# Optimization experiments

Measured on AMD Instinct MI355X. Metric: run time of the kernel, lower is better.

## Reference

```python
import jax, jax.numpy as jnp
import numpy as np

D_MODEL = 512
N_HEADS = 8
HEAD_DIM = D_MODEL // N_HEADS  # 64


def setup_inputs() -> dict:
    key = jax.random.key(0)
    ks = jax.random.split(key, 12)
    B, SQ, SK = 4, 2048, 2048
    s = 1.0 / np.sqrt(D_MODEL)
    return {
        "query": jax.random.normal(ks[0], (B, SQ, D_MODEL), jnp.float32),
        "key": jax.random.normal(ks[1], (B, SK, D_MODEL), jnp.float32),
        "value": jax.random.normal(ks[2], (B, SK, D_MODEL), jnp.float32),
        "Wq": jax.random.normal(ks[3], (D_MODEL, D_MODEL), jnp.float32) * s,
        "bq": jnp.zeros((D_MODEL,), jnp.float32),
        "Wk": jax.random.normal(ks[4], (D_MODEL, D_MODEL), jnp.float32) * s,
        "bk": jnp.zeros((D_MODEL,), jnp.float32),
        "Wv": jax.random.normal(ks[5], (D_MODEL, D_MODEL), jnp.float32) * s,
        "bv": jnp.zeros((D_MODEL,), jnp.float32),
        "Wo": jax.random.normal(ks[6], (D_MODEL, D_MODEL), jnp.float32) * s,
        "bo": jnp.zeros((D_MODEL,), jnp.float32),
    }


def reference(query, key, value, Wq, bq, Wk, bk, Wv, bv, Wo, bo):
    B, SQ, _ = query.shape
    SK = key.shape[1]
    # QKV projections
    Q = query @ Wq.T + bq  # [B,SQ,D]
    K = key @ Wk.T + bk    # [B,SK,D]
    V = value @ Wv.T + bv  # [B,SK,D]
    # split heads -> [B,H,S,hd]
    Q = Q.reshape(B, SQ, N_HEADS, HEAD_DIM).transpose(0, 2, 1, 3)
    K = K.reshape(B, SK, N_HEADS, HEAD_DIM).transpose(0, 2, 1, 3)
    V = V.reshape(B, SK, N_HEADS, HEAD_DIM).transpose(0, 2, 1, 3)
    scale = jnp.sqrt(jnp.float32(HEAD_DIM))
    scores = jnp.einsum('bhqd,bhkd->bhqk', Q, K) / scale  # [B,H,SQ,SK]
    attn = jax.nn.softmax(scores, axis=-1)  # dropout p=0 (eval)
    ctx = jnp.einsum('bhqk,bhkd->bhqd', attn, V)
    ctx = ctx.transpose(0, 2, 1, 3).reshape(B, SQ, D_MODEL)
    # exact (erf) GELU as in torch F.gelu default
    out = jax.nn.gelu(ctx, approximate=False) @ Wo.T + bo
    return out
```

## Files before the change

### kernel.cpp

```cpp
#include <hip/hip_runtime.h>
#include <hip/hip_bf16.h>

#define D_MODEL 512
#define N_HEADS 8
#define HEAD_DIM 64
#define BATCH 4
#define SEQ 2048

typedef _Float16 f16;
typedef _Float16 f16x8 __attribute__((ext_vector_type(8)));
typedef _Float16 f16x4 __attribute__((ext_vector_type(4)));
typedef float f32x4 __attribute__((ext_vector_type(4)));
typedef unsigned int u32x4 __attribute__((ext_vector_type(4)));

#define MFMA16(a, b, c) __builtin_amdgcn_mfma_f32_16x16x32_f16((a), (b), (c), 0, 0, 0)

#define GLOAD_LDS16(src, dst)                                                   \
    __builtin_amdgcn_global_load_lds(                                           \
        (const __attribute__((address_space(1))) void*)(src),                   \
        (__attribute__((address_space(3))) void*)(dst), 16, 0, 0)

#if __has_builtin(__builtin_amdgcn_exp2f)
#define EXP2(x) __builtin_amdgcn_exp2f(x)
#else
#define EXP2(x) __expf((x) * 0.6931471805599453f)
#endif

#define QSCALE 0.18033688011112042f
#define OFF2 8.656170245333781f

__global__ __launch_bounds__(256) void wsplit(
    const float* __restrict__ w0, const float* __restrict__ w1,
    const float* __restrict__ w2, const float* __restrict__ w3,
    f16* __restrict__ h0, f16* __restrict__ h1,
    f16* __restrict__ h2, f16* __restrict__ h3)
{
    const int j = blockIdx.y;
    const float* s = (j == 0) ? w0 : (j == 1) ? w1 : (j == 2) ? w2 : w3;
    f16* dh = (j == 0) ? h0 : (j == 1) ? h1 : (j == 2) ? h2 : h3;
    const int n4 = (D_MODEL * D_MODEL) >> 2;
    for (int i = blockIdx.x * 256 + threadIdx.x; i < n4; i += gridDim.x * 256) {
        float4 x = ((const float4*)s)[i];
        f16x4 hv = {(f16)x.x, (f16)x.y, (f16)x.z, (f16)x.w};
        ((f16x4*)dh)[i] = hv;
    }
}

__global__ __launch_bounds__(256, 3) void proj_mfma(
    const float* __restrict__ Xq, const float* __restrict__ Xk,
    const float* __restrict__ Xv,
    const f16* __restrict__ Wqh, const f16* __restrict__ Wkh,
    const f16* __restrict__ Wvh,
    const float* __restrict__ bq, const float* __restrict__ bk,
    const float* __restrict__ bv,
    f16* __restrict__ Qh, f16* __restrict__ Kh, f16* __restrict__ Vt)
{
    __shared__ f16 ldsA[128 * 64];
    __shared__ f16 ldsW[128 * 64];

    const int z = blockIdx.z;
    const float* X = (z == 0) ? Xq : (z == 1) ? Xk : Xv;
    const f16* Wh = (z == 0) ? Wqh : (z == 1) ? Wkh : Wvh;
    const float* bias = (z == 0) ? bq : (z == 1) ? bk : bv;

    const int m0 = blockIdx.x * 128;
    const int n0 = blockIdx.y * 128;

    const int tid = threadIdx.x;
    const int w = tid >> 6, l = tid & 63;
    const int lp = l >> 4, lq = l & 15;
    const int wm = w >> 1, wn = w & 1;

    f32x4 acc[4][4] = {};

    for (int kt = 0; kt < D_MODEL; kt += 64) {
        __syncthreads();
        float4 av[4][2];
        int arow[4], aslot[4];
#pragma unroll
        for (int j = 0; j < 4; ++j) {
            const int chunk = j * 256 + tid;
            arow[j] = chunk >> 3;
            aslot[j] = chunk & 7;
            const float* sp = X + (size_t)(m0 + arow[j]) * D_MODEL + kt + aslot[j] * 8;
            av[j][0] = *(const float4*)sp;
            av[j][1] = *(const float4*)(sp + 4);
        }
#pragma unroll
        for (int j = 0; j < 4; ++j) {
            const int cb = j * 256 + w * 64;
            const int chunk = cb + l;
            const int row = chunk >> 3;
            const int slot = (chunk & 7) ^ (row & 7);
            GLOAD_LDS16(Wh + (size_t)(n0 + row) * D_MODEL + kt + slot * 8,
                        ldsW + cb * 8);
        }
#pragma unroll
        for (int j = 0; j < 4; ++j) {
            f16x8 hv;
            hv[0] = (f16)av[j][0].x; hv[1] = (f16)av[j][0].y;
            hv[2] = (f16)av[j][0].z; hv[3] = (f16)av[j][0].w;
            hv[4] = (f16)av[j][1].x; hv[5] = (f16)av[j][1].y;
            hv[6] = (f16)av[j][1].z; hv[7] = (f16)av[j][1].w;
            *(f16x8*)(ldsA + arow[j] * 64 + ((aslot[j] ^ (arow[j] & 7)) << 3)) = hv;
        }
        __syncthreads();

        f16x8 af[4][2];
#pragma unroll
        for (int mt = 0; mt < 4; ++mt) {
            const int R = wm * 64 + mt * 16 + lq;
#pragma unroll
            for (int s = 0; s < 2; ++s)
                af[mt][s] = *(const f16x8*)(ldsA + R * 64 + (((s * 4 + lp) ^ (R & 7)) << 3));
        }
        __builtin_amdgcn_s_setprio(1);
#pragma unroll
        for (int nt = 0; nt < 4; ++nt) {
            const int R = wn * 64 + nt * 16 + lq;
            f16x8 b0 = *(const f16x8*)(ldsW + R * 64 + (((0 + lp) ^ (R & 7)) << 3));
            f16x8 b1 = *(const f16x8*)(ldsW + R * 64 + (((4 + lp) ^ (R & 7)) << 3));
#pragma unroll
            for (int mt = 0; mt < 4; ++mt) {
                acc[mt][nt] = MFMA16(af[mt][0], b0, acc[mt][nt]);
                acc[mt][nt] = MFMA16(af[mt][1], b1, acc[mt][nt]);
            }
        }
        __builtin_amdgcn_s_setprio(0);
    }

    const int m_base = m0 + wm * 64;
    const int n_base = n0 + wn * 64;
    const int b = m0 / SEQ;
    const int h = n_base >> 6;
    const size_t bh_ = (size_t)b * N_HEADS + h;

    if (z == 0) {
#pragma unroll
        for (int nt = 0; nt < 4; ++nt) {
            const int n = n_base + nt * 16 + lq;
            const float bn = bias[n];
            const int d = n & 63;
#pragma unroll
            for (int mt = 0; mt < 4; ++mt) {
#pragma unroll
                for (int r = 0; r < 4; ++r) {
                    const int s = (m_base + mt * 16 + lp * 4 + r) & (SEQ - 1);
                    Qh[(bh_ * SEQ + s) * 64 + d] = (f16)((acc[mt][nt][r] + bn) * QSCALE);
                }
            }
        }
    } else if (z == 1) {
#pragma unroll
        for (int nt = 0; nt < 4; ++nt) {
            const int n = n_base + nt * 16 + lq;
            const float bn = bias[n];
            const int d = n & 63;
#pragma unroll
            for (int mt = 0; mt < 4; ++mt) {
#pragma unroll
                for (int r = 0; r < 4; ++r) {
                    const int s = (m_base + mt * 16 + lp * 4 + r) & (SEQ - 1);
                    Kh[(bh_ * SEQ + s) * 64 + d] = (f16)(acc[mt][nt][r] + bn);
                }
            }
        }
    } else {
#pragma unroll
        for (int nt = 0; nt < 4; ++nt) {
            const int n = n_base + nt * 16 + lq;
            const float bn = bias[n];
            const int d = n & 63;
#pragma unroll
            for (int mt = 0; mt < 4; ++mt) {
                const int s0 = (m_base + mt * 16 + lp * 4) & (SEQ - 1);
                f16x4 col;
#pragma unroll
                for (int r = 0; r < 4; ++r)
                    col[r] = (f16)(acc[mt][nt][r] + bn);
                *(f16x4*)(Vt + (bh_ * 64 + d) * SEQ + s0) = col;
            }
        }
    }
}

__global__ __launch_bounds__(256, 4) void out_mfma(
    const f16* __restrict__ Gh, const f16* __restrict__ Woh,
    const float* __restrict__ bo, float* __restrict__ Out)
{
    __shared__ f16 ldsA[64 * 64];
    __shared__ f16 ldsW[128 * 64];

    const int m0 = blockIdx.x * 64;
    const int n0 = blockIdx.y * 128;

    const int tid = threadIdx.x;
    const int w = tid >> 6, l = tid & 63;
    const int lp = l >> 4, lq = l & 15;
    const int wm = w >> 1, wn = w & 1;

    f32x4 acc[2][4] = {};

    for (int kt = 0; kt < D_MODEL; kt += 64) {
        __syncthreads();
#pragma unroll
        for (int j = 0; j < 2; ++j) {
            const int cb = j * 256 + w * 64;
            const int chunk = cb + l;
            const int row = chunk >> 3;
            const int slot = (chunk & 7) ^ (row & 7);
            GLOAD_LDS16(Gh + (size_t)(m0 + row) * D_MODEL + kt + slot * 8,
                        ldsA + cb * 8);
        }
#pragma unroll
        for (int j = 0; j < 4; ++j) {
            const int cb = j * 256 + w * 64;
            const int chunk = cb + l;
            const int row = chunk >> 3;
            const int slot = (chunk & 7) ^ (row & 7);
            GLOAD_LDS16(Woh + (size_t)(n0 + row) * D_MODEL + kt + slot * 8,
                        ldsW + cb * 8);
        }
        __syncthreads();

        f16x8 af[2][2];
#pragma unroll
        for (int mt = 0; mt < 2; ++mt) {
            const int R = wm * 32 + mt * 16 + lq;
#pragma unroll
            for (int s = 0; s < 2; ++s)
                af[mt][s] = *(const f16x8*)(ldsA + R * 64 + (((s * 4 + lp) ^ (R & 7)) << 3));
        }
        __builtin_amdgcn_s_setprio(1);
#pragma unroll
        for (int nt = 0; nt < 4; ++nt) {
            const int R = wn * 64 + nt * 16 + lq;
            f16x8 b0 = *(const f16x8*)(ldsW + R * 64 + (((0 + lp) ^ (R & 7)) << 3));
            f16x8 b1 = *(const f16x8*)(ldsW + R * 64 + (((4 + lp) ^ (R & 7)) << 3));
#pragma unroll
            for (int mt = 0; mt < 2; ++mt) {
                acc[mt][nt] = MFMA16(af[mt][0], b0, acc[mt][nt]);
                acc[mt][nt] = MFMA16(af[mt][1], b1, acc[mt][nt]);
            }
        }
        __builtin_amdgcn_s_setprio(0);
    }

#pragma unroll
    for (int nt = 0; nt < 4; ++nt) {
        const int n = n0 + wn * 64 + nt * 16 + lq;
        const float bn = bo[n];
#pragma unroll
        for (int mt = 0; mt < 2; ++mt) {
#pragma unroll
            for (int r = 0; r < 4; ++r) {
                const int m = m0 + wm * 32 + mt * 16 + lp * 4 + r;
                Out[(size_t)m * D_MODEL + n] = acc[mt][nt][r] + bn;
            }
        }
    }
}

__global__ __launch_bounds__(256, 4) void flash_mfma(
    const f16* __restrict__ Qh, const f16* __restrict__ Kh,
    const f16* __restrict__ Vt, f16* __restrict__ Gh)
{
    __shared__ f16 KV[2][2][4096];

    const int tid = threadIdx.x;
    const int w  = tid >> 6;
    const int l  = tid & 63;
    const int lp = l >> 4;
    const int lq = l & 15;

    const int id = blockIdx.x;
    const int work = (id & 7) * 128 + (id >> 3);
    const int bh = work >> 5;
    const int b  = bh >> 3, h = bh & 7;
    const int qw = (work & 31) * 64 + w * 16;

    f16x8 qf[2];
#pragma unroll
    for (int s = 0; s < 2; ++s)
        qf[s] = *(const f16x8*)(Qh + ((size_t)bh * SEQ + qw + lq) * 64 + s * 32 + lp * 8);

    f16x8 ones;
#pragma unroll
    for (int i = 0; i < 8; ++i) ones[i] = (f16)1.f;

    f32x4 o[4];
#pragma unroll
    for (int c = 0; c < 4; ++c) o[c] = (f32x4){0.f, 0.f, 0.f, 0.f};
    f32x4 lf = (f32x4){0.f, 0.f, 0.f, 0.f};

    auto STAGE = [&](int k0, int bf) {
#pragma unroll
        for (int j = 0; j < 4; ++j) {
            const int gi = w + 4 * j;
            const int tset = gi >> 3;
            const int t = gi & 7;
            const int lrow = t * 8 + (l >> 3);
            const int slot = (l & 7) ^ (lrow & 7);
            if (tset == 0)
                GLOAD_LDS16(Kh + ((size_t)bh * SEQ + k0 + lrow) * 64 + slot * 8,
                            &KV[bf][0][t * 512]);
            else
                GLOAD_LDS16(Vt + ((size_t)bh * 64 + lrow) * SEQ + k0 + slot * 8,
                            &KV[bf][1][t * 512]);
        }
    };

    STAGE(0, 0);
    int buf = 0;
    const int NT = SEQ / 64;

    for (int t = 0; t < NT; ++t) {
        asm volatile("s_waitcnt vmcnt(0)" ::: "memory");
        __builtin_amdgcn_s_barrier();
        if (t < NT - 1) STAGE((t + 1) * 64, buf ^ 1);
        __builtin_amdgcn_sched_barrier(0);

        const f16* Kt_ = &KV[buf][0][0];
        const f16* Vt_ = &KV[buf][1][0];

        f32x4 st[4];
#pragma unroll
        for (int c = 0; c < 4; ++c)
            st[c] = (f32x4){-OFF2, -OFF2, -OFF2, -OFF2};
        __builtin_amdgcn_s_setprio(1);
#pragma unroll
        for (int mt = 0; mt < 4; ++mt) {
            const int krow = mt * 16 + lq;
#pragma unroll
            for (int s = 0; s < 2; ++s) {
                const int byteoff = krow * 128 + (((4 * s + lp) ^ (krow & 7)) << 4);
                f16x8 ah = *(const f16x8*)((const char*)Kt_ + byteoff);
                st[mt] = MFMA16(ah, qf[s], st[mt]);
            }
        }
        __builtin_amdgcn_s_setprio(0);

        f16x8 vbr[2][4];
#pragma unroll
        for (int s = 0; s < 2; ++s)
#pragma unroll
            for (int nt = 0; nt < 4; ++nt) {
                const int d = nt * 16 + lq;
                const int byteoff = d * 128 + (((4 * s + lp) ^ (d & 7)) << 4);
                vbr[s][nt] = *(const f16x8*)((const char*)Vt_ + byteoff);
            }

        unsigned int pk0[4], pk1[4];
#pragma unroll
        for (int mt = 0; mt < 4; ++mt) {
            float e0 = EXP2(st[mt][0]);
            float e1 = EXP2(st[mt][1]);
            float e2 = EXP2(st[mt][2]);
            float e3 = EXP2(st[mt][3]);
            pk0[mt] = __builtin_bit_cast(unsigned int,
                          __builtin_amdgcn_cvt_pkrtz(e0, e1));
            pk1[mt] = __builtin_bit_cast(unsigned int,
                          __builtin_amdgcn_cvt_pkrtz(e2, e3));
        }

        f16x8 pa[2];
#pragma unroll
        for (int s = 0; s < 2; ++s) {
            unsigned int x0 = pk0[2 * s], y0 = pk0[2 * s + 1];
            unsigned int x1 = pk1[2 * s], y1 = pk1[2 * s + 1];
            asm("v_permlane32_swap_b32 %0, %1" : "+v"(x0), "+v"(y0));
            asm("v_permlane16_swap_b32 %0, %1" : "+v"(x0), "+v"(y0));
            asm("v_permlane32_swap_b32 %0, %1" : "+v"(x1), "+v"(y1));
            asm("v_permlane16_swap_b32 %0, %1" : "+v"(x1), "+v"(y1));
            u32x4 t4 = {x0, x1, y0, y1};
            pa[s] = __builtin_bit_cast(f16x8, t4);
        }

        __builtin_amdgcn_s_setprio(1);
#pragma unroll
        for (int s = 0; s < 2; ++s) {
            lf = MFMA16(pa[s], ones, lf);
#pragma unroll
            for (int nt = 0; nt < 4; ++nt)
                o[nt] = MFMA16(pa[s], vbr[s][nt], o[nt]);
        }
        __builtin_amdgcn_s_setprio(0);

        buf ^= 1;
    }

#pragma unroll
    for (int j = 0; j < 4; ++j) {
        const float inv = 1.f / lf[j];
        const int row = qw + lp * 4 + j;
#pragma unroll
        for (int nt = 0; nt < 4; ++nt) {
            float x = o[nt][j] * inv;
            float g = 0.5f * x * (1.f + erff(x * 0.70710678118654752f));
            Gh[((size_t)(b * SEQ + row)) * D_MODEL + h * 64 + nt * 16 + lq] = (f16)g;
        }
    }
}

extern "C" void kernel_launch(void* const* d_in, const int* in_sizes, int n_in,
                              void* d_out, int out_size, void* d_ws, size_t ws_size,
                              hipStream_t stream)
{
    const float* query = (const float*)d_in[0];
    const float* key   = (const float*)d_in[1];
    const float* value = (const float*)d_in[2];
    const float* Wq = (const float*)d_in[3];
    const float* bq = (const float*)d_in[4];
    const float* Wk = (const float*)d_in[5];
    const float* bk = (const float*)d_in[6];
    const float* Wv = (const float*)d_in[7];
    const float* bv = (const float*)d_in[8];
    const float* Wo = (const float*)d_in[9];
    const float* bo = (const float*)d_in[10];

    char* ws = (char*)d_ws;
    const size_t MB = 1024 * 1024;
    const size_t KB = 1024;
    f16* Qh = (f16*)(ws + 0 * MB);
    f16* Kh = (f16*)(ws + 8 * MB);
    f16* Vt = (f16*)(ws + 16 * MB);
    f16* Gh = (f16*)(ws + 24 * MB);
    f16* Wqh = (f16*)(ws + 32 * MB);
    f16* Wkh = (f16*)(ws + 32 * MB + 512 * KB);
    f16* Wvh = (f16*)(ws + 33 * MB);
    f16* Woh = (f16*)(ws + 33 * MB + 512 * KB);

    wsplit<<<dim3(64, 4), 256, 0, stream>>>(Wq, Wk, Wv, Wo, Wqh, Wkh, Wvh, Woh);

    proj_mfma<<<dim3(BATCH * SEQ / 128, D_MODEL / 128, 3), 256, 0, stream>>>(
        query, key, value, Wqh, Wkh, Wvh, bq, bk, bv, Qh, Kh, Vt);

    flash_mfma<<<dim3(1024), 256, 0, stream>>>(Qh, Kh, Vt, Gh);

    out_mfma<<<dim3(BATCH * SEQ / 64, D_MODEL / 128), 256, 0, stream>>>(
        Gh, Woh, bo, (float*)d_out);
}
```

Baseline: 93.17 us.

## Process two 16-row query sub-tiles per wave in flash attention

Each wave now handles 32 query rows as two 16-row sub-tiles instead of 16, so a block covers 128 queries and the grid shrinks from 1024 to 512 blocks. Each K fragment and V fragment read from LDS is reused for two MFMAs, halving LDS traffic and K/V global staging per query row. In exchange, register pressure roughly doubles for accumulators, launch bounds drop to 2 blocks per SM, and fewer blocks may reduce latency hiding and load balance across the 256 CUs.

```diff
diff --git a/kernel.cpp b/kernel.cpp
--- a/kernel.cpp
+++ b/kernel.cpp
@@ -261,7 +261,7 @@
     }
 }
 
-__global__ __launch_bounds__(256, 4) void flash_mfma(
+__global__ __launch_bounds__(256, 2) void flash_mfma(
     const f16* __restrict__ Qh, const f16* __restrict__ Kh,
     const f16* __restrict__ Vt, f16* __restrict__ Gh)
 {
@@ -274,24 +274,29 @@
     const int lq = l & 15;
 
     const int id = blockIdx.x;
-    const int work = (id & 7) * 128 + (id >> 3);
-    const int bh = work >> 5;
+    const int work = (id & 7) * 64 + (id >> 3);
+    const int bh = work >> 4;
     const int b  = bh >> 3, h = bh & 7;
-    const int qw = (work & 31) * 64 + w * 16;
-
-    f16x8 qf[2];
-#pragma unroll
-    for (int s = 0; s < 2; ++s)
-        qf[s] = *(const f16x8*)(Qh + ((size_t)bh * SEQ + qw + lq) * 64 + s * 32 + lp * 8);
+    const int q0 = (work & 15) * 128 + w * 32;
+
+    f16x8 qf[2][2];
+#pragma unroll
+    for (int sub = 0; sub < 2; ++sub)
+#pragma unroll
+        for (int s = 0; s < 2; ++s)
+            qf[sub][s] = *(const f16x8*)(Qh + ((size_t)bh * SEQ + q0 + sub * 16 + lq) * 64
+                                          + s * 32 + lp * 8);
 
     f16x8 ones;
 #pragma unroll
     for (int i = 0; i < 8; ++i) ones[i] = (f16)1.f;
 
-    f32x4 o[4];
-#pragma unroll
-    for (int c = 0; c < 4; ++c) o[c] = (f32x4){0.f, 0.f, 0.f, 0.f};
-    f32x4 lf = (f32x4){0.f, 0.f, 0.f, 0.f};
+    f32x4 o[2][4];
+#pragma unroll
+    for (int sub = 0; sub < 2; ++sub)
+#pragma unroll
+        for (int c = 0; c < 4; ++c) o[sub][c] = (f32x4){0.f, 0.f, 0.f, 0.f};
+    f32x4 lf[2] = {(f32x4){0.f, 0.f, 0.f, 0.f}, (f32x4){0.f, 0.f, 0.f, 0.f}};
 
     auto STAGE = [&](int k0, int bf) {
 #pragma unroll
@@ -323,10 +328,12 @@
         const f16* Kt_ = &KV[buf][0][0];
         const f16* Vt_ = &KV[buf][1][0];
 
-        f32x4 st[4];
-#pragma unroll
-        for (int c = 0; c < 4; ++c)
-            st[c] = (f32x4){-OFF2, -OFF2, -OFF2, -OFF2};
+        f32x4 st[2][4];
+#pragma unroll
+        for (int sub = 0; sub < 2; ++sub)
+#pragma unroll
+            for (int c = 0; c < 4; ++c)
+                st[sub][c] = (f32x4){-OFF2, -OFF2, -OFF2, -OFF2};
         __builtin_amdgcn_s_setprio(1);
 #pragma unroll
         for (int mt = 0; mt < 4; ++mt) {
@@ -335,7 +342,9 @@
             for (int s = 0; s < 2; ++s) {
                 const int byteoff = krow * 128 + (((4 * s + lp) ^ (krow & 7)) << 4);
                 f16x8 ah = *(const f16x8*)((const char*)Kt_ + byteoff);
-                st[mt] = MFMA16(ah, qf[s], st[mt]);
+#pragma unroll
+                for (int sub = 0; sub < 2; ++sub)
+                    st[sub][mt] = MFMA16(ah, qf[sub][s], st[sub][mt]);
             }
         }
         __builtin_amdgcn_s_setprio(0);
@@ -350,39 +359,44 @@
                 vbr[s][nt] = *(const f16x8*)((const char*)Vt_ + byteoff);
             }
 
-        unsigned int pk0[4], pk1[4];
-#pragma unroll
-        for (int mt = 0; mt < 4; ++mt) {
-            float e0 = EXP2(st[mt][0]);
-            float e1 = EXP2(st[mt][1]);
-            float e2 = EXP2(st[mt][2]);
-            float e3 = EXP2(st[mt][3]);
-            pk0[mt] = __builtin_bit_cast(unsigned int,
-                          __builtin_amdgcn_cvt_pkrtz(e0, e1));
-            pk1[mt] = __builtin_bit_cast(unsigned int,
-                          __builtin_amdgcn_cvt_pkrtz(e2, e3));
-        }
-
-        f16x8 pa[2];
+        f16x8 pa[2][2];
+#pragma unroll
+        for (int sub = 0; sub < 2; ++sub) {
+            unsigned int pk0[4], pk1[4];
+#pragma unroll
+            for (int mt = 0; mt < 4; ++mt) {
+                float e0 = EXP2(st[sub][mt][0]);
+                float e1 = EXP2(st[sub][mt][1]);
+                float e2 = EXP2(st[sub][mt][2]);
+                float e3 = EXP2(st[sub][mt][3]);
+                pk0[mt] = __builtin_bit_cast(unsigned int,
+                              __builtin_amdgcn_cvt_pkrtz(e0, e1));
+                pk1[mt] = __builtin_bit_cast(unsigned int,
+                              __builtin_amdgcn_cvt_pkrtz(e2, e3));
+            }
+#pragma unroll
+            for (int s = 0; s < 2; ++s) {
+                unsigned int x0 = pk0[2 * s], y0 = pk0[2 * s + 1];
+                unsigned int x1 = pk1[2 * s], y1 = pk1[2 * s + 1];
+                asm("v_permlane32_swap_b32 %0, %1" : "+v"(x0), "+v"(y0));
+                asm("v_permlane16_swap_b32 %0, %1" : "+v"(x0), "+v"(y0));
+                asm("v_permlane32_swap_b32 %0, %1" : "+v"(x1), "+v"(y1));
+                asm("v_permlane16_swap_b32 %0, %1" : "+v"(x1), "+v"(y1));
+                u32x4 t4 = {x0, x1, y0, y1};
+                pa[sub][s] = __builtin_bit_cast(f16x8, t4);
+            }
+        }
+
+        __builtin_amdgcn_s_setprio(1);
 #pragma unroll
         for (int s = 0; s < 2; ++s) {
-            unsigned int x0 = pk0[2 * s], y0 = pk0[2 * s + 1];
-            unsigned int x1 = pk1[2 * s], y1 = pk1[2 * s + 1];
-            asm("v_permlane32_swap_b32 %0, %1" : "+v"(x0), "+v"(y0));
-            asm("v_permlane16_swap_b32 %0, %1" : "+v"(x0), "+v"(y0));
-            asm("v_permlane32_swap_b32 %0, %1" : "+v"(x1), "+v"(y1));
-            asm("v_permlane16_swap_b32 %0, %1" : "+v"(x1), "+v"(y1));
-            u32x4 t4 = {x0, x1, y0, y1};
-            pa[s] = __builtin_bit_cast(f16x8, t4);
-        }
-
-        __builtin_amdgcn_s_setprio(1);
-#pragma unroll
-        for (int s = 0; s < 2; ++s) {
-            lf = MFMA16(pa[s], ones, lf);
-#pragma unroll
-            for (int nt = 0; nt < 4; ++nt)
-                o[nt] = MFMA16(pa[s], vbr[s][nt], o[nt]);
+#pragma unroll
+            for (int sub = 0; sub < 2; ++sub) {
+                lf[sub] = MFMA16(pa[sub][s], ones, lf[sub]);
+#pragma unroll
+                for (int nt = 0; nt < 4; ++nt)
+                    o[sub][nt] = MFMA16(pa[sub][s], vbr[s][nt], o[sub][nt]);
+            }
         }
         __builtin_amdgcn_s_setprio(0);
 
@@ -390,14 +404,17 @@
     }
 
 #pragma unroll
-    for (int j = 0; j < 4; ++j) {
-        const float inv = 1.f / lf[j];
-        const int row = qw + lp * 4 + j;
-#pragma unroll
-        for (int nt = 0; nt < 4; ++nt) {
-            float x = o[nt][j] * inv;
-            float g = 0.5f * x * (1.f + erff(x * 0.70710678118654752f));
-            Gh[((size_t)(b * SEQ + row)) * D_MODEL + h * 64 + nt * 16 + lq] = (f16)g;
+    for (int sub = 0; sub < 2; ++sub) {
+#pragma unroll
+        for (int j = 0; j < 4; ++j) {
+            const float inv = 1.f / lf[sub][j];
+            const int row = q0 + sub * 16 + lp * 4 + j;
+#pragma unroll
+            for (int nt = 0; nt < 4; ++nt) {
+                float x = o[sub][nt][j] * inv;
+                float g = 0.5f * x * (1.f + erff(x * 0.70710678118654752f));
+                Gh[((size_t)(b * SEQ + row)) * D_MODEL + h * 64 + nt * 16 + lq] = (f16)g;
+            }
         }
     }
 }
@@ -435,7 +452,7 @@
     proj_mfma<<<dim3(BATCH * SEQ / 128, D_MODEL / 128, 3), 256, 0, stream>>>(
         query, key, value, Wqh, Wkh, Wvh, bq, bk, bv, Qh, Kh, Vt);
 
-    flash_mfma<<<dim3(1024), 256, 0, stream>>>(Qh, Kh, Vt, Gh);
+    flash_mfma<<<dim3(512), 256, 0, stream>>>(Qh, Kh, Vt, Gh);
 
     out_mfma<<<dim3(BATCH * SEQ / 64, D_MODEL / 128), 256, 0, stream>>>(
         Gh, Woh, bo, (float*)d_out);
```

Measured after the change: 85.79 us. 7.9% less time.
